# Performance work log

Measured on AMD Instinct MI355X. Metric: run time of the kernel, lower is better.

Reference implementation:

```python
import jax, jax.numpy as jnp
import numpy as np

HEADS = 8
DIM_HEAD = 64
QUERY_DIM = 1024
CONTEXT_DIM = 768
INNER = HEADS * DIM_HEAD  # 512


def setup_inputs() -> dict:
    key = jax.random.key(0)
    ks = jax.random.split(key, 7)
    B, Sq, Skv = 4, 4096, 1024
    x = jax.random.normal(ks[0], (B, Sq, QUERY_DIM), dtype=jnp.float32)
    context = jax.random.normal(ks[1], (B, Skv, CONTEXT_DIM), dtype=jnp.float32)
    # nn.Linear(in, out) weights stored as [out, in]; we use [in, out] for x @ W
    Wq = jax.random.normal(ks[2], (QUERY_DIM, INNER), dtype=jnp.float32) * (QUERY_DIM ** -0.5)
    Wk = jax.random.normal(ks[3], (CONTEXT_DIM, INNER), dtype=jnp.float32) * (CONTEXT_DIM ** -0.5)
    Wv = jax.random.normal(ks[4], (CONTEXT_DIM, INNER), dtype=jnp.float32) * (CONTEXT_DIM ** -0.5)
    Wo = jax.random.normal(ks[5], (INNER, QUERY_DIM), dtype=jnp.float32) * (INNER ** -0.5)
    bo = jax.random.normal(ks[6], (QUERY_DIM,), dtype=jnp.float32) * 0.01
    return {"x": x, "context": context, "Wq": Wq, "Wk": Wk, "Wv": Wv, "Wo": Wo, "bo": bo}


def reference(x, context, Wq, Wk, Wv, Wo, bo):
    B, Sq, _ = x.shape
    h, d = HEADS, DIM_HEAD
    scale = d ** -0.5
    # project and split heads: [B, S, h*d] -> [B, h, S, d]
    q = (x @ Wq).reshape(B, Sq, h, d).transpose(0, 2, 1, 3)
    k = (context @ Wk).reshape(B, -1, h, d).transpose(0, 2, 1, 3)
    v = (context @ Wv).reshape(B, -1, h, d).transpose(0, 2, 1, 3)
    # the torch chunked loop is exactly full softmax attention (softmax is row-wise)
    scores = jnp.einsum('bhid,bhjd->bhij', q, k) * scale
    attn = jax.nn.softmax(scores, axis=-1)
    out = jnp.einsum('bhij,bhjd->bhid', attn, v)  # [B, h, Sq, d]
    out = out.transpose(0, 2, 1, 3).reshape(B, Sq, h * d)
    return out @ Wo + bo
```

## Files before the change

kernel.cpp:

```cpp
#include <hip/hip_runtime.h>

#define SQ 4096
#define SKV 1024
#define BATCH 4
#define NH 8
#define DH 64
#define QD 1024
#define CD 768
#define INNER 512

typedef _Float16 half8 __attribute__((ext_vector_type(8)));
typedef _Float16 half4v __attribute__((ext_vector_type(4)));
typedef float floatx4 __attribute__((ext_vector_type(4)));
typedef float f32x16 __attribute__((ext_vector_type(16)));
typedef unsigned int uint4v __attribute__((ext_vector_type(4)));

#define MFMA16(a, b, c) __builtin_amdgcn_mfma_f32_16x16x32_f16(a, b, c, 0, 0, 0)
#define MFMA32(a, b, c) __builtin_amdgcn_mfma_f32_32x32x16_f16(a, b, c, 0, 0, 0)

#define PLSWAP(a, b) asm("v_permlane32_swap_b32 %0, %1" : "+v"(a), "+v"(b))

#define GLD16(gptr, lptr)                                                            \
  __builtin_amdgcn_global_load_lds(                                                  \
      (const __attribute__((address_space(1))) unsigned int*)(const void*)(gptr),    \
      (__attribute__((address_space(3))) unsigned int*)(void*)(lptr), 16, 0, 0)

__global__ __launch_bounds__(256) void prep(const float* __restrict__ x,
                                            const float* __restrict__ ctx,
                                            const float* __restrict__ Wq,
                                            const float* __restrict__ Wk,
                                            const float* __restrict__ Wv,
                                            const float* __restrict__ Wo,
                                            _Float16* __restrict__ xh,
                                            _Float16* __restrict__ ctxh,
                                            _Float16* __restrict__ wqt,
                                            _Float16* __restrict__ wkvt,
                                            _Float16* __restrict__ wot) {
  __shared__ float tile[32][33];
  const size_t NX = (size_t)BATCH * SQ * QD;
  const size_t NC = (size_t)BATCH * SKV * CD;
  const unsigned NCAST = (unsigned)((NX + NC) / 2048);

  if (blockIdx.x < NCAST) {
    size_t i = ((size_t)blockIdx.x * 256 + threadIdx.x) * 8;
    const float* s;
    _Float16* d;
    size_t off;
    if (i < NX) { s = x; d = xh; off = i; }
    else        { s = ctx; d = ctxh; off = i - NX; }
    floatx4 a = *(const floatx4*)(s + off);
    floatx4 b = *(const floatx4*)(s + off + 4);
    half8 h;
#pragma unroll
    for (int j = 0; j < 4; ++j) { h[j] = (_Float16)a[j]; h[4 + j] = (_Float16)b[j]; }
    *(half8*)(d + off) = h;
    return;
  }
  const unsigned t = blockIdx.x - NCAST;
  const int z = t >> 10, rem = t & 1023;
  const float* src; _Float16* dst; int R, C;
  if (z == 0)      { src = Wq; dst = wqt;                        R = QD;    C = INNER; }
  else if (z == 1) { src = Wk; dst = wkvt;                       R = CD;    C = INNER; }
  else if (z == 2) { src = Wv; dst = wkvt + (size_t)INNER * CD;  R = CD;    C = INNER; }
  else             { src = Wo; dst = wot;                        R = INNER; C = QD;   }
  const int c0 = (rem & 31) * 32, r0 = (rem >> 5) * 32;
  if (c0 >= C || r0 >= R) return;
  const int tx = threadIdx.x & 31, ty = threadIdx.x >> 5;
#pragma unroll
  for (int i = 0; i < 32; i += 8)
    tile[ty + i][tx] = src[(size_t)(r0 + ty + i) * C + c0 + tx];
  __syncthreads();
#pragma unroll
  for (int i = 0; i < 32; i += 8)
    dst[(size_t)(c0 + ty + i) * R + r0 + tx] = (_Float16)tile[tx][ty + i];
}

template <int MODE>
__device__ __forceinline__ void gemm_body(const _Float16* __restrict__ A,
                                          const _Float16* __restrict__ Bt,
                                          void* __restrict__ Cout,
                                          void* __restrict__ Cout2,
                                          const float* __restrict__ bias,
                                          int M, int N, int K, int bx, int by,
                                          _Float16* As16, _Float16* Bs) {
  const int tid = threadIdx.x;
  const int wave = tid >> 6, lane = tid & 63;
  const int quad = lane >> 4, l16 = lane & 15;
  const int wm = (wave >> 1) * 64, wn = (wave & 1) * 64;
  const size_t n0 = (size_t)bx * 128, m0 = (size_t)by * 128;

  floatx4 acc[4][4] = {};

  const int a16r = tid >> 2, a16b = (tid & 3) ^ ((a16r >> 1) & 3);
  const _Float16* ag = A + (m0 + a16r) * (size_t)K + a16b * 8;
  const _Float16* bg = Bt + (n0 + a16r) * (size_t)K + a16b * 8;

#define GSTAGE(bi, k0)                                                      \
  do {                                                                      \
    GLD16(ag + (k0), As16 + (bi)*4096 + tid * 8);                           \
    GLD16(ag + (k0) + (size_t)64 * K, As16 + (bi)*4096 + tid * 8 + 2048);   \
    GLD16(bg + (k0), Bs + (bi)*4096 + tid * 8);                             \
    GLD16(bg + (k0) + (size_t)64 * K, Bs + (bi)*4096 + tid * 8 + 2048);     \
  } while (0)

  const int NT = K / 32;
  GSTAGE(0, 0);
  GSTAGE(1, 32);
  int cb = 0;
  for (int t = 0; t < NT; ++t) {
    if (t + 1 < NT)
      asm volatile("s_waitcnt vmcnt(4)" ::: "memory");
    else
      asm volatile("s_waitcnt vmcnt(0)" ::: "memory");
    __builtin_amdgcn_sched_barrier(0);
    __builtin_amdgcn_s_barrier();
    __builtin_amdgcn_sched_barrier(0);
    if (t + 2 < NT) {
      int nb = cb + 2; if (nb >= 3) nb -= 3;
      GSTAGE(nb, (t + 2) * 32);
    }
    const _Float16* as = As16 + cb * 4096;
    const _Float16* bs = Bs + cb * 4096;

    const int r2 = (l16 >> 1) & 3;
    half8 af[4], bf[4];
#pragma unroll
    for (int mt = 0; mt < 4; ++mt)
      af[mt] = *(const half8*)(as + (wm + mt * 16 + l16) * 32 + (quad ^ r2) * 8);
#pragma unroll
    for (int nt = 0; nt < 4; ++nt)
      bf[nt] = *(const half8*)(bs + (wn + nt * 16 + l16) * 32 + (quad ^ r2) * 8);
    __builtin_amdgcn_s_setprio(1);
#pragma unroll
    for (int mt = 0; mt < 4; ++mt)
#pragma unroll
      for (int nt = 0; nt < 4; ++nt)
        acc[mt][nt] = MFMA16(af[mt], bf[nt], acc[mt][nt]);
    __builtin_amdgcn_s_setprio(0);
    cb = (cb == 2) ? 0 : cb + 1;
  }
#undef GSTAGE

  if (MODE == 3) {
    _Float16* C = (_Float16*)Cout;
    const float sc = 0.125f * 1.44269504088896f;
#pragma unroll
    for (int mt = 0; mt < 4; ++mt) {
      const size_t row = m0 + wm + mt * 16 + quad * 4;
#pragma unroll
      for (int nt = 0; nt < 4; ++nt) {
        const size_t col = n0 + wn + nt * 16 + l16;
#pragma unroll
        for (int r = 0; r < 4; ++r)
          C[(row + r) * N + col] = (_Float16)(acc[mt][nt][r] * sc);
      }
    }
  } else if (MODE == 4) {
    if (n0 < INNER) {
      _Float16* C = (_Float16*)Cout;
#pragma unroll
      for (int mt = 0; mt < 4; ++mt) {
        const size_t row = m0 + wm + mt * 16 + quad * 4;
#pragma unroll
        for (int nt = 0; nt < 4; ++nt) {
          const size_t col = n0 + wn + nt * 16 + l16;
#pragma unroll
          for (int r = 0; r < 4; ++r)
            C[(row + r) * INNER + col] = (_Float16)acc[mt][nt][r];
        }
      }
    } else {
      _Float16* C = (_Float16*)Cout2;
      const int b = (int)(m0 >> 10);
#pragma unroll
      for (int mt = 0; mt < 4; ++mt) {
        const int kvb = (int)(m0 & 1023) + wm + mt * 16 + quad * 4;
#pragma unroll
        for (int nt = 0; nt < 4; ++nt) {
          const int col = (int)(n0 - INNER + wn + nt * 16 + l16);
          const int h = col >> 6, d = col & 63;
          half4v pk;
#pragma unroll
          for (int r = 0; r < 4; ++r) pk[r] = (_Float16)acc[mt][nt][r];
          *(half4v*)(C + (size_t)((b * NH + h) * DH + d) * SKV + kvb) = pk;
        }
      }
    }
  } else {
    float* C = (float*)Cout;
#pragma unroll
    for (int mt = 0; mt < 4; ++mt) {
      const size_t row = m0 + wm + mt * 16 + quad * 4;
#pragma unroll
      for (int nt = 0; nt < 4; ++nt) {
        const size_t col = n0 + wn + nt * 16 + l16;
        const float bb = bias[col];
#pragma unroll
        for (int r = 0; r < 4; ++r)
          C[(row + r) * N + col] = acc[mt][nt][r] + bb;
      }
    }
  }
}

__global__ __launch_bounds__(256) void proj_fused(const _Float16* __restrict__ xh,
                                                  const _Float16* __restrict__ ctxh,
                                                  const _Float16* __restrict__ wqt,
                                                  const _Float16* __restrict__ wkvt,
                                                  _Float16* __restrict__ qh,
                                                  _Float16* __restrict__ kh,
                                                  _Float16* __restrict__ vth) {
  __shared__ _Float16 As16[3 * 128 * 32];
  __shared__ _Float16 Bs[3 * 128 * 32];
  const int b = blockIdx.x;
  const int xcd = b & 7, j = b >> 3;
  const int seg = j % 3;
  if (seg == 2) {
    const int jkv = j / 3;
    gemm_body<4>(ctxh, wkvt, kh, vth, nullptr, BATCH * SKV, 2 * INNER, CD,
                 jkv & 7, xcd * 4 + (jkv >> 3), As16, Bs);
  } else {
    const int jq = (j / 3) * 2 + seg;
    gemm_body<3>(xh, wqt, qh, nullptr, nullptr, BATCH * SQ, INNER, QD,
                 jq & 3, xcd * 16 + (jq >> 2), As16, Bs);
  }
}

__global__ __launch_bounds__(256) void gemm_out(const _Float16* __restrict__ A,
                                                const _Float16* __restrict__ Bt,
                                                float* __restrict__ Cout,
                                                const float* __restrict__ bias) {
  __shared__ _Float16 As16[3 * 128 * 32];
  __shared__ _Float16 Bs[3 * 128 * 32];
  const int b = blockIdx.x;
  const int xcd = b & 7, i = b >> 3;
  gemm_body<2>(A, Bt, Cout, nullptr, bias, BATCH * SQ, QD, INNER,
               i & 7, xcd * 16 + (i >> 3), As16, Bs);
}

__global__ __launch_bounds__(256, 3) void flash_attn8(const _Float16* __restrict__ Q,
                                                      const _Float16* __restrict__ Kp,
                                                      const _Float16* __restrict__ Vt,
                                                      _Float16* __restrict__ O) {
  __shared__ _Float16 Ksb[2 * 64 * 64];
  __shared__ _Float16 Vsb[2 * 64 * 64];
  const int tid = threadIdx.x;
  const int wave = tid >> 6, lane = tid & 63;
  const int l31 = lane & 31, hi = lane >> 5, x7 = lane & 7;

  const int flat = blockIdx.x;
  const int nf = (flat & 7) * 128 + (flat >> 3);
  const int qblk = nf & 31, bh = nf >> 5;
  const int b = bh >> 3, h = bh & 7;

  const size_t qrow0 = (size_t)b * SQ + qblk * 128 + wave * 32;
  const _Float16* qptr = Q + qrow0 * INNER + h * DH;
  const _Float16* kbase = Kp + (size_t)b * SKV * INNER + h * DH;
  const _Float16* vbase = Vt + (size_t)bh * DH * SKV;

  const int kr = tid >> 3;
  const int kb = (tid & 7) ^ (kr & 7);
  const _Float16* kg = kbase + (size_t)kr * INNER + kb * 8;
  const _Float16* vg = vbase + (size_t)kr * SKV + kb * 8;

#define STAGE_KV(bi, tt)                                                        \
  do {                                                                          \
    _Float16* _kl = Ksb + (bi) * 4096 + tid * 8;                                \
    _Float16* _vl = Vsb + (bi) * 4096 + tid * 8;                                \
    GLD16(kg + (size_t)((tt) * 64) * INNER, _kl);                               \
    GLD16(kg + (size_t)((tt) * 64 + 32) * INNER, _kl + 2048);                   \
    GLD16(vg + (tt) * 64, _vl);                                                 \
    GLD16(vg + (size_t)32 * SKV + (tt) * 64, _vl + 2048);                       \
  } while (0)

  half8 aq[4];
#pragma unroll
  for (int i = 0; i < 4; ++i)
    aq[i] = *(const half8*)(qptr + (size_t)l31 * INNER + i * 16 + hi * 8);

  int koff[4], voffB[4];
#pragma unroll
  for (int i = 0; i < 4; ++i)
    koff[i] = l31 * 64 + (((i * 2 + hi) ^ x7) << 3);
#pragma unroll
  for (int j = 0; j < 4; ++j)
    voffB[j] = l31 * 64 + (((j * 2 + hi) ^ x7) << 3);

  half8 ones;
#pragma unroll
  for (int j = 0; j < 8; ++j) ones[j] = (_Float16)1.0f;

  f32x16 o0 = {}, o1 = {}, osum = {};

  STAGE_KV(0, 0);

  for (int t = 0; t < SKV / 64; ++t) {
    __syncthreads();
    if (t < SKV / 64 - 1) STAGE_KV((t + 1) & 1, t + 1);
    const _Float16* ks = Ksb + (t & 1) * 4096;
    const _Float16* vs = Vsb + (t & 1) * 4096;

#pragma unroll
    for (int c2 = 0; c2 < 2; ++c2) {
      half8 ak[4];
#pragma unroll
      for (int i = 0; i < 4; ++i)
        ak[i] = *(const half8*)(ks + c2 * 2048 + koff[i]);

      f32x16 st = {};
#pragma unroll
      for (int i = 0; i < 4; ++i) st = MFMA32(ak[i], aq[i], st);

      unsigned w[8];
#pragma unroll
      for (int j = 0; j < 8; ++j) {
        float plo = __builtin_exp2f(st[2 * j]);
        float phi = __builtin_exp2f(st[2 * j + 1]);
        w[j] = __builtin_bit_cast(unsigned, __builtin_amdgcn_cvt_pkrtz(plo, phi));
      }
      PLSWAP(w[0], w[2]);
      PLSWAP(w[1], w[3]);
      PLSWAP(w[4], w[6]);
      PLSWAP(w[5], w[7]);
      uint4v u0 = {w[0], w[1], w[2], w[3]};
      uint4v u1 = {w[4], w[5], w[6], w[7]};
      half8 A0 = __builtin_bit_cast(half8, u0);
      half8 A1 = __builtin_bit_cast(half8, u1);

      osum = MFMA32(A0, ones, osum);
      osum = MFMA32(A1, ones, osum);

      {
        half8 bv00 = *(const half8*)(vs + 0 * 2048 + voffB[c2 * 2 + 0]);
        half8 bv10 = *(const half8*)(vs + 1 * 2048 + voffB[c2 * 2 + 0]);
        o0 = MFMA32(A0, bv00, o0);
        o1 = MFMA32(A0, bv10, o1);
        half8 bv01 = *(const half8*)(vs + 0 * 2048 + voffB[c2 * 2 + 1]);
        half8 bv11 = *(const half8*)(vs + 1 * 2048 + voffB[c2 * 2 + 1]);
        o0 = MFMA32(A1, bv01, o0);
        o1 = MFMA32(A1, bv11, o1);
      }
    }
  }

  float inv16[16];
#pragma unroll
  for (int r = 0; r < 16; ++r) inv16[r] = 1.0f / osum[r];

  _Float16* op = O + qrow0 * INNER + h * DH;
#pragma unroll
  for (int r = 0; r < 16; ++r) {
    const int q = (r & 3) + 8 * (r >> 2) + 4 * hi;
    op[(size_t)q * INNER + l31] = (_Float16)(o0[r] * inv16[r]);
    op[(size_t)q * INNER + 32 + l31] = (_Float16)(o1[r] * inv16[r]);
  }
#undef STAGE_KV
}

extern "C" void kernel_launch(void* const* d_in, const int* in_sizes, int n_in,
                              void* d_out, int out_size, void* d_ws, size_t ws_size,
                              hipStream_t stream) {
  const float* x   = (const float*)d_in[0];
  const float* ctx = (const float*)d_in[1];
  const float* Wq  = (const float*)d_in[2];
  const float* Wk  = (const float*)d_in[3];
  const float* Wv  = (const float*)d_in[4];
  const float* Wo  = (const float*)d_in[5];
  const float* bo  = (const float*)d_in[6];
  float* out = (float*)d_out;

  const size_t NX = (size_t)BATCH * SQ * QD;
  const size_t NC = (size_t)BATCH * SKV * CD;

  _Float16* ws = (_Float16*)d_ws;
  _Float16* xh   = ws;
  _Float16* ctxh = xh + NX;
  _Float16* wqt  = ctxh + NC;
  _Float16* wkvt = wqt + (size_t)INNER * QD;
  _Float16* wot  = wkvt + (size_t)2 * INNER * CD;
  _Float16* qh   = wot + (size_t)QD * INNER;
  _Float16* kh   = qh + (size_t)BATCH * SQ * INNER;
  _Float16* vth  = kh + (size_t)BATCH * SKV * INNER;
  _Float16* aoh  = xh;

  prep<<<dim3((unsigned)((NX + NC) / 2048) + 4096), 256, 0, stream>>>(
      x, ctx, Wq, Wk, Wv, Wo, xh, ctxh, wqt, wkvt, wot);

  proj_fused<<<dim3(768), 256, 0, stream>>>(xh, ctxh, wqt, wkvt, qh, kh, vth);

  flash_attn8<<<dim3(BATCH * NH * SQ / 128), 256, 0, stream>>>(qh, kh, vth, aoh);

  gemm_out<<<dim3(1024), 256, 0, stream>>>(aoh, wot, out, bo);
}
```

Before: 257.8 us.

## Enlarge output GEMM tile to 256x128 with 512 threads, template GEMM sizes

The output projection GEMM becomes a standalone kernel with a 256x128 block tile computed by 8 waves (512 threads), halving the block count and sharing each B tile across twice as many rows. The shared gemm_body now takes K and N as template constants with a partially unrolled k-loop, and flash attention's launch bounds request 4 blocks per SM instead of 3. The larger tile cuts redundant B loads but uses more LDS per block. The tighter occupancy hint on attention may force register spills.

```diff
diff --git a/kernel.cpp b/kernel.cpp
--- a/kernel.cpp
+++ b/kernel.cpp
@@ -75,13 +75,12 @@
     dst[(size_t)(c0 + ty + i) * R + r0 + tx] = (_Float16)tile[tx][ty + i];
 }
 
-template <int MODE>
+template <int MODE, int K, int N>
 __device__ __forceinline__ void gemm_body(const _Float16* __restrict__ A,
                                           const _Float16* __restrict__ Bt,
                                           void* __restrict__ Cout,
                                           void* __restrict__ Cout2,
-                                          const float* __restrict__ bias,
-                                          int M, int N, int K, int bx, int by,
+                                          int bx, int by,
                                           _Float16* As16, _Float16* Bs) {
   const int tid = threadIdx.x;
   const int wave = tid >> 6, lane = tid & 63;
@@ -103,10 +102,11 @@
     GLD16(bg + (k0) + (size_t)64 * K, Bs + (bi)*4096 + tid * 8 + 2048);     \
   } while (0)
 
-  const int NT = K / 32;
+  constexpr int NT = K / 32;
   GSTAGE(0, 0);
   GSTAGE(1, 32);
   int cb = 0;
+#pragma unroll 2
   for (int t = 0; t < NT; ++t) {
     if (t + 1 < NT)
       asm volatile("s_waitcnt vmcnt(4)" ::: "memory");
@@ -184,20 +184,6 @@
           for (int r = 0; r < 4; ++r) pk[r] = (_Float16)acc[mt][nt][r];
           *(half4v*)(C + (size_t)((b * NH + h) * DH + d) * SKV + kvb) = pk;
         }
-      }
-    }
-  } else {
-    float* C = (float*)Cout;
-#pragma unroll
-    for (int mt = 0; mt < 4; ++mt) {
-      const size_t row = m0 + wm + mt * 16 + quad * 4;
-#pragma unroll
-      for (int nt = 0; nt < 4; ++nt) {
-        const size_t col = n0 + wn + nt * 16 + l16;
-        const float bb = bias[col];
-#pragma unroll
-        for (int r = 0; r < 4; ++r)
-          C[(row + r) * N + col] = acc[mt][nt][r] + bb;
       }
     }
   }
@@ -217,28 +203,99 @@
   const int seg = j % 3;
   if (seg == 2) {
     const int jkv = j / 3;
-    gemm_body<4>(ctxh, wkvt, kh, vth, nullptr, BATCH * SKV, 2 * INNER, CD,
-                 jkv & 7, xcd * 4 + (jkv >> 3), As16, Bs);
+    gemm_body<4, CD, 2 * INNER>(ctxh, wkvt, kh, vth,
+                                jkv & 7, xcd * 4 + (jkv >> 3), As16, Bs);
   } else {
     const int jq = (j / 3) * 2 + seg;
-    gemm_body<3>(xh, wqt, qh, nullptr, nullptr, BATCH * SQ, INNER, QD,
-                 jq & 3, xcd * 16 + (jq >> 2), As16, Bs);
-  }
-}
-
-__global__ __launch_bounds__(256) void gemm_out(const _Float16* __restrict__ A,
+    gemm_body<3, QD, INNER>(xh, wqt, qh, nullptr,
+                            jq & 3, xcd * 16 + (jq >> 2), As16, Bs);
+  }
+}
+
+__global__ __launch_bounds__(512) void gemm_out(const _Float16* __restrict__ A,
                                                 const _Float16* __restrict__ Bt,
                                                 float* __restrict__ Cout,
                                                 const float* __restrict__ bias) {
-  __shared__ _Float16 As16[3 * 128 * 32];
+  constexpr int K = INNER;
+  constexpr int N = QD;
+  __shared__ _Float16 As16[3 * 256 * 32];
   __shared__ _Float16 Bs[3 * 128 * 32];
+  const int tid = threadIdx.x;
+  const int wave = tid >> 6, lane = tid & 63;
+  const int quad = lane >> 4, l16 = lane & 15;
+  const int wm = (wave >> 1) * 64, wn = (wave & 1) * 64;
   const int b = blockIdx.x;
   const int xcd = b & 7, i = b >> 3;
-  gemm_body<2>(A, Bt, Cout, nullptr, bias, BATCH * SQ, QD, INNER,
-               i & 7, xcd * 16 + (i >> 3), As16, Bs);
-}
-
-__global__ __launch_bounds__(256, 3) void flash_attn8(const _Float16* __restrict__ Q,
+  const int bx = i & 7, by = xcd * 8 + (i >> 3);
+  const size_t n0 = (size_t)bx * 128, m0 = (size_t)by * 256;
+
+  floatx4 acc[4][4] = {};
+
+  const int r4 = tid >> 2, b4 = (tid & 3) ^ ((r4 >> 1) & 3);
+  const _Float16* ag = A + (m0 + r4) * (size_t)K + b4 * 8;
+  const _Float16* bg = Bt + (n0 + r4) * (size_t)K + b4 * 8;
+
+#define GSTAGE2(bi, k0)                                                    \
+  do {                                                                     \
+    GLD16(ag + (k0), As16 + (bi)*8192 + tid * 8);                          \
+    GLD16(ag + (k0) + (size_t)128 * K, As16 + (bi)*8192 + tid * 8 + 4096); \
+    GLD16(bg + (k0), Bs + (bi)*4096 + tid * 8);                            \
+  } while (0)
+
+  constexpr int NT = K / 32;
+  GSTAGE2(0, 0);
+  GSTAGE2(1, 32);
+  int cb = 0;
+#pragma unroll 2
+  for (int t = 0; t < NT; ++t) {
+    if (t + 1 < NT)
+      asm volatile("s_waitcnt vmcnt(3)" ::: "memory");
+    else
+      asm volatile("s_waitcnt vmcnt(0)" ::: "memory");
+    __builtin_amdgcn_sched_barrier(0);
+    __builtin_amdgcn_s_barrier();
+    __builtin_amdgcn_sched_barrier(0);
+    if (t + 2 < NT) {
+      int nb = cb + 2; if (nb >= 3) nb -= 3;
+      GSTAGE2(nb, (t + 2) * 32);
+    }
+    const _Float16* as = As16 + cb * 8192;
+    const _Float16* bs = Bs + cb * 4096;
+
+    const int r2 = (l16 >> 1) & 3;
+    half8 af[4], bf[4];
+#pragma unroll
+    for (int mt = 0; mt < 4; ++mt)
+      af[mt] = *(const half8*)(as + (wm + mt * 16 + l16) * 32 + (quad ^ r2) * 8);
+#pragma unroll
+    for (int nt = 0; nt < 4; ++nt)
+      bf[nt] = *(const half8*)(bs + (wn + nt * 16 + l16) * 32 + (quad ^ r2) * 8);
+    __builtin_amdgcn_s_setprio(1);
+#pragma unroll
+    for (int mt = 0; mt < 4; ++mt)
+#pragma unroll
+      for (int nt = 0; nt < 4; ++nt)
+        acc[mt][nt] = MFMA16(af[mt], bf[nt], acc[mt][nt]);
+    __builtin_amdgcn_s_setprio(0);
+    cb = (cb == 2) ? 0 : cb + 1;
+  }
+#undef GSTAGE2
+
+#pragma unroll
+  for (int mt = 0; mt < 4; ++mt) {
+    const size_t row = m0 + wm + mt * 16 + quad * 4;
+#pragma unroll
+    for (int nt = 0; nt < 4; ++nt) {
+      const size_t col = n0 + wn + nt * 16 + l16;
+      const float bb = bias[col];
+#pragma unroll
+      for (int r = 0; r < 4; ++r)
+        Cout[(row + r) * N + col] = acc[mt][nt][r] + bb;
+    }
+  }
+}
+
+__global__ __launch_bounds__(256, 4) void flash_attn8(const _Float16* __restrict__ Q,
                                                       const _Float16* __restrict__ Kp,
                                                       const _Float16* __restrict__ Vt,
                                                       _Float16* __restrict__ O) {
@@ -390,5 +447,5 @@
 
   flash_attn8<<<dim3(BATCH * NH * SQ / 128), 256, 0, stream>>>(qh, kh, vth, aoh);
 
-  gemm_out<<<dim3(1024), 256, 0, stream>>>(aoh, wot, out, bo);
-}
+  gemm_out<<<dim3(512), 512, 0, stream>>>(aoh, wot, out, bo);
+}
```

After: 250.3 us. -2.9%, faster.

## Enlarge projection and output GEMM tiles to 256x128 with 512-thread blocks

Applied to the files above, without the earlier changes.

Replaces the 128x128 GEMM body with a 256x128 variant that runs on 512-thread blocks (eight waves). It specialises K and N as template parameters and unrolls the main loop by two. Each block now loads one B tile for twice as many A rows, which cuts B-tile global traffic and halves the block count for the projection and output GEMMs. The flash attention kernel's launch bound is raised to request four blocks per CU instead of three. The costs are more LDS per block, which may lower GEMM occupancy, and more register pressure from the stricter attention bound.

```diff
diff --git a/kernel.cpp b/kernel.cpp
--- a/kernel.cpp
+++ b/kernel.cpp
@@ -75,41 +75,41 @@
     dst[(size_t)(c0 + ty + i) * R + r0 + tx] = (_Float16)tile[tx][ty + i];
 }
 
-template <int MODE>
-__device__ __forceinline__ void gemm_body(const _Float16* __restrict__ A,
-                                          const _Float16* __restrict__ Bt,
-                                          void* __restrict__ Cout,
-                                          void* __restrict__ Cout2,
-                                          const float* __restrict__ bias,
-                                          int M, int N, int K, int bx, int by,
-                                          _Float16* As16, _Float16* Bs) {
+template <int MODE, int K, int N>
+__device__ __forceinline__ void gemm256_body(const _Float16* __restrict__ A,
+                                             const _Float16* __restrict__ Bt,
+                                             void* __restrict__ Cout,
+                                             void* __restrict__ Cout2,
+                                             const float* __restrict__ bias,
+                                             int bx, int by,
+                                             _Float16* As16, _Float16* Bs) {
   const int tid = threadIdx.x;
   const int wave = tid >> 6, lane = tid & 63;
   const int quad = lane >> 4, l16 = lane & 15;
   const int wm = (wave >> 1) * 64, wn = (wave & 1) * 64;
-  const size_t n0 = (size_t)bx * 128, m0 = (size_t)by * 128;
+  const size_t n0 = (size_t)bx * 128, m0 = (size_t)by * 256;
 
   floatx4 acc[4][4] = {};
 
-  const int a16r = tid >> 2, a16b = (tid & 3) ^ ((a16r >> 1) & 3);
-  const _Float16* ag = A + (m0 + a16r) * (size_t)K + a16b * 8;
-  const _Float16* bg = Bt + (n0 + a16r) * (size_t)K + a16b * 8;
-
-#define GSTAGE(bi, k0)                                                      \
-  do {                                                                      \
-    GLD16(ag + (k0), As16 + (bi)*4096 + tid * 8);                           \
-    GLD16(ag + (k0) + (size_t)64 * K, As16 + (bi)*4096 + tid * 8 + 2048);   \
-    GLD16(bg + (k0), Bs + (bi)*4096 + tid * 8);                             \
-    GLD16(bg + (k0) + (size_t)64 * K, Bs + (bi)*4096 + tid * 8 + 2048);     \
+  const int r4 = tid >> 2, b4 = (tid & 3) ^ ((r4 >> 1) & 3);
+  const _Float16* ag = A + (m0 + r4) * (size_t)K + b4 * 8;
+  const _Float16* bg = Bt + (n0 + r4) * (size_t)K + b4 * 8;
+
+#define GSTAGE2(bi, k0)                                                    \
+  do {                                                                     \
+    GLD16(ag + (k0), As16 + (bi)*8192 + tid * 8);                          \
+    GLD16(ag + (k0) + (size_t)128 * K, As16 + (bi)*8192 + tid * 8 + 4096); \
+    GLD16(bg + (k0), Bs + (bi)*4096 + tid * 8);                            \
   } while (0)
 
-  const int NT = K / 32;
-  GSTAGE(0, 0);
-  GSTAGE(1, 32);
+  constexpr int NT = K / 32;
+  GSTAGE2(0, 0);
+  GSTAGE2(1, 32);
   int cb = 0;
+#pragma unroll 2
   for (int t = 0; t < NT; ++t) {
     if (t + 1 < NT)
-      asm volatile("s_waitcnt vmcnt(4)" ::: "memory");
+      asm volatile("s_waitcnt vmcnt(3)" ::: "memory");
     else
       asm volatile("s_waitcnt vmcnt(0)" ::: "memory");
     __builtin_amdgcn_sched_barrier(0);
@@ -117,9 +117,9 @@
     __builtin_amdgcn_sched_barrier(0);
     if (t + 2 < NT) {
       int nb = cb + 2; if (nb >= 3) nb -= 3;
-      GSTAGE(nb, (t + 2) * 32);
-    }
-    const _Float16* as = As16 + cb * 4096;
+      GSTAGE2(nb, (t + 2) * 32);
+    }
+    const _Float16* as = As16 + cb * 8192;
     const _Float16* bs = Bs + cb * 4096;
 
     const int r2 = (l16 >> 1) & 3;
@@ -139,7 +139,7 @@
     __builtin_amdgcn_s_setprio(0);
     cb = (cb == 2) ? 0 : cb + 1;
   }
-#undef GSTAGE
+#undef GSTAGE2
 
   if (MODE == 3) {
     _Float16* C = (_Float16*)Cout;
@@ -203,42 +203,42 @@
   }
 }
 
-__global__ __launch_bounds__(256) void proj_fused(const _Float16* __restrict__ xh,
+__global__ __launch_bounds__(512) void proj_fused(const _Float16* __restrict__ xh,
                                                   const _Float16* __restrict__ ctxh,
                                                   const _Float16* __restrict__ wqt,
                                                   const _Float16* __restrict__ wkvt,
                                                   _Float16* __restrict__ qh,
                                                   _Float16* __restrict__ kh,
                                                   _Float16* __restrict__ vth) {
-  __shared__ _Float16 As16[3 * 128 * 32];
+  __shared__ _Float16 As16[3 * 256 * 32];
   __shared__ _Float16 Bs[3 * 128 * 32];
   const int b = blockIdx.x;
   const int xcd = b & 7, j = b >> 3;
   const int seg = j % 3;
   if (seg == 2) {
     const int jkv = j / 3;
-    gemm_body<4>(ctxh, wkvt, kh, vth, nullptr, BATCH * SKV, 2 * INNER, CD,
-                 jkv & 7, xcd * 4 + (jkv >> 3), As16, Bs);
+    gemm256_body<4, CD, 2 * INNER>(ctxh, wkvt, kh, vth, nullptr,
+                                   jkv & 7, xcd * 2 + (jkv >> 3), As16, Bs);
   } else {
     const int jq = (j / 3) * 2 + seg;
-    gemm_body<3>(xh, wqt, qh, nullptr, nullptr, BATCH * SQ, INNER, QD,
-                 jq & 3, xcd * 16 + (jq >> 2), As16, Bs);
-  }
-}
-
-__global__ __launch_bounds__(256) void gemm_out(const _Float16* __restrict__ A,
+    gemm256_body<3, QD, INNER>(xh, wqt, qh, nullptr, nullptr,
+                               jq & 3, xcd * 8 + (jq >> 2), As16, Bs);
+  }
+}
+
+__global__ __launch_bounds__(512) void gemm_out(const _Float16* __restrict__ A,
                                                 const _Float16* __restrict__ Bt,
                                                 float* __restrict__ Cout,
                                                 const float* __restrict__ bias) {
-  __shared__ _Float16 As16[3 * 128 * 32];
+  __shared__ _Float16 As16[3 * 256 * 32];
   __shared__ _Float16 Bs[3 * 128 * 32];
   const int b = blockIdx.x;
   const int xcd = b & 7, i = b >> 3;
-  gemm_body<2>(A, Bt, Cout, nullptr, bias, BATCH * SQ, QD, INNER,
-               i & 7, xcd * 16 + (i >> 3), As16, Bs);
-}
-
-__global__ __launch_bounds__(256, 3) void flash_attn8(const _Float16* __restrict__ Q,
+  gemm256_body<2, INNER, QD>(A, Bt, Cout, nullptr, bias,
+                             i & 7, xcd * 8 + (i >> 3), As16, Bs);
+}
+
+__global__ __launch_bounds__(256, 4) void flash_attn8(const _Float16* __restrict__ Q,
                                                       const _Float16* __restrict__ Kp,
                                                       const _Float16* __restrict__ Vt,
                                                       _Float16* __restrict__ O) {
@@ -386,9 +386,9 @@
   prep<<<dim3((unsigned)((NX + NC) / 2048) + 4096), 256, 0, stream>>>(
       x, ctx, Wq, Wk, Wv, Wo, xh, ctxh, wqt, wkvt, wot);
 
-  proj_fused<<<dim3(768), 256, 0, stream>>>(xh, ctxh, wqt, wkvt, qh, kh, vth);
+  proj_fused<<<dim3(384), 512, 0, stream>>>(xh, ctxh, wqt, wkvt, qh, kh, vth);
 
   flash_attn8<<<dim3(BATCH * NH * SQ / 128), 256, 0, stream>>>(qh, kh, vth, aoh);
 
-  gemm_out<<<dim3(1024), 256, 0, stream>>>(aoh, wot, out, bo);
-}
+  gemm_out<<<dim3(512), 512, 0, stream>>>(aoh, wot, out, bo);
+}
```

Result: no change. 257.8 us (+0.0%).
